# Kernel optimization log

Measured on AMD Instinct MI355X. Metric: run time of the kernel, lower is better.

Reference implementation:

```python
import jax, jax.numpy as jnp
import numpy as np

D_MODEL = 1024
N_HEADS = 16
D_HEAD = D_MODEL // N_HEADS
B, S = 4, 2048


def setup_inputs() -> dict:
    key = jax.random.key(0)
    ks = jax.random.split(key, 12)
    std = 1.0 / np.sqrt(D_MODEL)
    inp = {
        "q": jax.random.normal(ks[0], (B, S, D_MODEL), jnp.float32),
        "k": jax.random.normal(ks[1], (B, S, D_MODEL), jnp.float32),
        "v": jax.random.normal(ks[2], (B, S, D_MODEL), jnp.float32),
        # causal mask: 1 where attention is disallowed (j > i)
        "mask": jnp.triu(jnp.ones((S, S), jnp.int32), k=1)[None, None],
        "Wq": jax.random.normal(ks[3], (D_MODEL, D_MODEL), jnp.float32) * std,
        "bq": jnp.zeros((D_MODEL,), jnp.float32),
        "Wk": jax.random.normal(ks[4], (D_MODEL, D_MODEL), jnp.float32) * std,
        "bk": jnp.zeros((D_MODEL,), jnp.float32),
        "Wv": jax.random.normal(ks[5], (D_MODEL, D_MODEL), jnp.float32) * std,
        "bv": jnp.zeros((D_MODEL,), jnp.float32),
        "Wo": jax.random.normal(ks[6], (D_MODEL, D_MODEL), jnp.float32) * std,
        "bo": jnp.zeros((D_MODEL,), jnp.float32),
    }
    return inp


def _split_heads(x):
    # [B, S, D] -> [B, H, S, d_head]
    b, s, _ = x.shape
    return x.reshape(b, s, N_HEADS, D_HEAD).transpose(0, 2, 1, 3)


def reference(q, k, v, mask, Wq, bq, Wk, bk, Wv, bv, Wo, bo):
    # torch Linear: y = x @ W.T + b
    qh = _split_heads(q @ Wq.T + bq)
    kh = _split_heads(k @ Wk.T + bk)
    vh = _split_heads(v @ Wv.T + bv)
    # NOTE: original scales by sqrt(d_model), not sqrt(d_head)
    scale = 1.0 / np.sqrt(D_MODEL).astype(np.float32)
    logits = jnp.einsum("bhqd,bhkd->bhqk", qh, kh) * scale
    logits = logits + mask.astype(logits.dtype) * (-1e9)
    weights = jax.nn.softmax(logits, axis=-1)
    attn = jnp.einsum("bhqk,bhkd->bhqd", weights, vh)
    attn = attn.transpose(0, 2, 1, 3).reshape(q.shape[0], -1, D_MODEL)
    out = attn @ Wo.T + bo
    return out, weights
```

## Files before the change

### kernel.cpp

```cpp
#include <hip/hip_runtime.h>
#include <stdint.h>

typedef unsigned short u16;
typedef __attribute__((ext_vector_type(8))) short bf16x8;
typedef __attribute__((ext_vector_type(8))) unsigned short us8;
typedef __attribute__((ext_vector_type(4))) float f32x4;

typedef __attribute__((address_space(1))) void as1_void;
typedef __attribute__((address_space(3))) void as3_void;

#define S_LEN 2048
#define DMODEL 1024
#define DH 64
#define NHEADS 16
#define NB 4
#define GM (NB * S_LEN)
#define GN DMODEL
#define GK DMODEL
#define SCALE 0.03125f

__device__ __forceinline__ void gload16(const void* g, void* l) {
  __builtin_amdgcn_global_load_lds((const as1_void*)g, (as3_void*)l, 16, 0, 0);
}
__device__ __forceinline__ float bf2f(u16 u) {
  union { unsigned int i; float f; } x; x.i = ((unsigned int)u) << 16; return x.f;
}
__device__ __forceinline__ u16 f2bf(float f) {
  union { float f; unsigned int i; } x; x.f = f;
  unsigned int u = x.i + 0x7fffu + ((x.i >> 16) & 1u);
  return (u16)(u >> 16);
}
__device__ __forceinline__ f32x4 mfma16(bf16x8 a, bf16x8 b, f32x4 c) {
  return __builtin_amdgcn_mfma_f32_16x16x32_bf16(a, b, c, 0, 0, 0);
}
__device__ __forceinline__ void nt_store4(f32x4 v, float* p) {
  __builtin_nontemporal_store(v, (f32x4*)p);
}

__device__ __forceinline__ void cvt_chunk(const float* s, u16* d, int i) {
  const f32x4 a = *(const f32x4*)(s + (size_t)i * 8);
  const f32x4 b = *(const f32x4*)(s + (size_t)i * 8 + 4);
  us8 o;
  o[0] = f2bf(a[0]); o[1] = f2bf(a[1]); o[2] = f2bf(a[2]); o[3] = f2bf(a[3]);
  o[4] = f2bf(b[0]); o[5] = f2bf(b[1]); o[6] = f2bf(b[2]); o[7] = f2bf(b[3]);
  *(us8*)(d + (size_t)i * 8) = o;
}
__global__ __launch_bounds__(256)
void cvt3(const float* __restrict__ s0, const float* __restrict__ s1,
          const float* __restrict__ s2, u16* __restrict__ d0,
          u16* __restrict__ d1, u16* __restrict__ d2, int n8) {
  const int i = blockIdx.x * 256 + threadIdx.x;
  if (i >= n8) return;
  const float* s; u16* d;
  if (blockIdx.y == 0)      { s = s0; d = d0; }
  else if (blockIdx.y == 1) { s = s1; d = d1; }
  else                      { s = s2; d = d2; }
  cvt_chunk(s, d, i);
}
__global__ __launch_bounds__(256)
void cvt4(const float* __restrict__ s0, const float* __restrict__ s1,
          const float* __restrict__ s2, const float* __restrict__ s3,
          u16* __restrict__ d0, u16* __restrict__ d1,
          u16* __restrict__ d2, u16* __restrict__ d3, int n8) {
  const int i = blockIdx.x * 256 + threadIdx.x;
  if (i >= n8) return;
  const float* s; u16* d;
  if (blockIdx.y == 0)      { s = s0; d = d0; }
  else if (blockIdx.y == 1) { s = s1; d = d1; }
  else if (blockIdx.y == 2) { s = s2; d = d2; }
  else                      { s = s3; d = d3; }
  cvt_chunk(s, d, i);
}

__device__ __forceinline__ void zero_tiles(float* __restrict__ wz, int tid,
                                           int t0, int bh_base, int tmax,
                                           int stride) {
  const f32x4 z4 = {0.f, 0.f, 0.f, 0.f};
  for (int t = t0; t < tmax; t += stride) {
    const int bh = bh_base + t / 120;
    int r = t % 120;
    int i = 0;
    while (r >= 15 - i) { r -= 15 - i; ++i; }
    const int j = i + 1 + r;
    float* p = wz + ((size_t)(bh * 2048 + i * 128)) * 2048 + j * 128;
#pragma unroll 4
    for (int c = tid; c < 4096; c += 256)
      nt_store4(z4, p + (size_t)(c >> 5) * 2048 + ((c & 31) << 2));
  }
}

#define GEMM_IDX                                                              \
  const int tid  = threadIdx.x;                                               \
  const int lane = tid & 63;                                                  \
  const int wvi  = tid >> 6;                                                  \
  const int wr   = wvi >> 1, wc = wvi & 1;                                    \
  const int rlow = lane & 15, rhi = lane >> 4;

#define GEMM_COMPUTE(Ab, Bb)                                                  \
  {                                                                           \
    bf16x8 af[4][2], bfr[4][2];                                               \
    _Pragma("unroll")                                                         \
    for (int mi = 0; mi < 4; ++mi) {                                          \
      const int row = wr * 64 + mi * 16 + rlow;                               \
      _Pragma("unroll")                                                       \
      for (int k2 = 0; k2 < 2; ++k2)                                          \
        af[mi][k2] = *(const bf16x8*)&(Ab)[row * 64 +                         \
                     (((rhi + k2 * 4) ^ (row & 7)) << 3)];                    \
    }                                                                         \
    _Pragma("unroll")                                                         \
    for (int ni = 0; ni < 4; ++ni) {                                          \
      const int row = wc * 64 + ni * 16 + rlow;                               \
      _Pragma("unroll")                                                       \
      for (int k2 = 0; k2 < 2; ++k2)                                          \
        bfr[ni][k2] = *(const bf16x8*)&(Bb)[row * 64 +                        \
                      (((rhi + k2 * 4) ^ (row & 7)) << 3)];                   \
    }                                                                         \
    _Pragma("unroll")                                                         \
    for (int mi = 0; mi < 4; ++mi)                                            \
      _Pragma("unroll")                                                       \
      for (int ni = 0; ni < 4; ++ni) {                                        \
        acc[mi][ni] = mfma16(af[mi][0], bfr[ni][0], acc[mi][ni]);             \
        acc[mi][ni] = mfma16(af[mi][1], bfr[ni][1], acc[mi][ni]);             \
      }                                                                       \
  }

#define ZSPLIT 5800

__global__ __launch_bounds__(256, 3)
void gemm_qkv(const u16* __restrict__ xq, const u16* __restrict__ xk,
              const u16* __restrict__ xv, const u16* __restrict__ wq,
              const u16* __restrict__ wk, const u16* __restrict__ wv,
              const float* __restrict__ bq, const float* __restrict__ bk,
              const float* __restrict__ bv, u16* __restrict__ oq,
              u16* __restrict__ ok, u16* __restrict__ ov,
              float* __restrict__ wz) {
  __shared__ u16 smem[2 * 8192];
  u16* As = smem;
  u16* Bs = smem + 8192;
  const u16 *A, *W; const float* bias; u16* C;
  if (blockIdx.z == 0)      { A = xq; W = wq; bias = bq; C = oq; }
  else if (blockIdx.z == 1) { A = xk; W = wk; bias = bk; C = ok; }
  else                      { A = xv; W = wv; bias = bv; C = ov; }
  GEMM_IDX
  const int m0 = blockIdx.x * 128;
  const int n0 = blockIdx.y * 128;

  f32x4 acc[4][4];
#pragma unroll
  for (int i = 0; i < 4; ++i)
#pragma unroll
    for (int j = 0; j < 4; ++j) acc[i][j] = (f32x4){0.f, 0.f, 0.f, 0.f};

  const int nk = GK >> 6;
  for (int kk = 0; kk < nk; ++kk) {
#pragma unroll
    for (int i = 0; i < 4; ++i) {
      const int c = i * 256 + tid;
      const int row = c >> 3, cw = c & 7;
      const int koff = (kk << 6) + ((cw ^ (row & 7)) << 3);
      gload16(A + (size_t)(m0 + row) * GK + koff, &As[(c - lane) << 3]);
      gload16(W + (size_t)(n0 + row) * GK + koff, &Bs[(c - lane) << 3]);
    }
    __syncthreads();
    GEMM_COMPUTE(As, Bs)
    __syncthreads();
  }

  {
    u16* Cs = smem;
#pragma unroll
    for (int ni = 0; ni < 4; ++ni) {
      const int col = wc * 64 + ni * 16 + rlow;
      const float bv2 = bias[n0 + col];
#pragma unroll
      for (int mi = 0; mi < 4; ++mi)
#pragma unroll
        for (int r = 0; r < 4; ++r)
          Cs[(wr * 64 + mi * 16 + rhi * 4 + r) * 128 + col] = f2bf(acc[mi][ni][r] + bv2);
    }
    __syncthreads();
#pragma unroll
    for (int i = 0; i < 8; ++i) {
      const int c = i * 256 + tid;
      const int row = c >> 4, cw = c & 15;
      const us8 t = *(const us8*)&Cs[row * 128 + cw * 8];
      *(us8*)&C[(size_t)(m0 + row) * GN + n0 + cw * 8] = t;
    }
  }

  {
    const int fid = blockIdx.x + blockIdx.y * 64 + blockIdx.z * 512;
    zero_tiles(wz, tid, fid, 3, ZSPLIT, 1536);
  }
}

__global__ __launch_bounds__(256, 2)
void gemm_o(const u16* __restrict__ A, const u16* __restrict__ W,
            const float* __restrict__ bias, float* __restrict__ C,
            float* __restrict__ wz) {
  __shared__ u16 smem[4 * 8192];
  u16* As = smem;
  u16* Bs = smem + 2 * 8192;
  GEMM_IDX
  const int m0 = blockIdx.x * 128;
  const int n0 = blockIdx.y * 128;

  f32x4 acc[4][4];
#pragma unroll
  for (int i = 0; i < 4; ++i)
#pragma unroll
    for (int j = 0; j < 4; ++j) acc[i][j] = (f32x4){0.f, 0.f, 0.f, 0.f};

#define STAGE_G(bufi, kk)                                                     \
  {                                                                           \
    _Pragma("unroll")                                                         \
    for (int i = 0; i < 4; ++i) {                                             \
      const int c = i * 256 + tid;                                            \
      const int row = c >> 3, cw = c & 7;                                     \
      const int koff = ((kk) << 6) + ((cw ^ (row & 7)) << 3);                 \
      gload16(A + (size_t)(m0 + row) * GK + koff,                             \
              &As[(bufi) * 8192 + ((c - lane) << 3)]);                        \
      gload16(W + (size_t)(n0 + row) * GK + koff,                             \
              &Bs[(bufi) * 8192 + ((c - lane) << 3)]);                        \
    }                                                                         \
  }

  const int nk = GK >> 6;
  STAGE_G(0, 0);
  __syncthreads();
  int buf = 0;
  for (int kk = 0; kk < nk; ++kk) {
    if (kk + 1 < nk) STAGE_G(buf ^ 1, kk + 1);
    const u16* Ab = &As[buf * 8192];
    const u16* Bb = &Bs[buf * 8192];
    GEMM_COMPUTE(Ab, Bb)
    __syncthreads();
    buf ^= 1;
  }
#undef STAGE_G

  {
    float* Cs = (float*)smem;
#pragma unroll
    for (int ni = 0; ni < 4; ++ni) {
      const int col = wc * 64 + ni * 16 + rlow;
      const float bv2 = bias[n0 + col];
#pragma unroll
      for (int mi = 0; mi < 4; ++mi)
#pragma unroll
        for (int r = 0; r < 4; ++r)
          Cs[(wr * 64 + mi * 16 + rhi * 4 + r) * 128 + col] = acc[mi][ni][r] + bv2;
    }
    __syncthreads();
#pragma unroll
    for (int i = 0; i < 16; ++i) {
      const int c = i * 256 + tid;
      const int row = c >> 5, cw = c & 31;
      const f32x4 t = *(const f32x4*)&Cs[row * 128 + cw * 4];
      nt_store4(t, &C[(size_t)(m0 + row) * GN + n0 + cw * 4]);
    }
  }

  {
    const int fid = blockIdx.x + blockIdx.y * 64;
    zero_tiles(wz, tid, ZSPLIT + fid, 3, 7320, 512);
    zero_tiles(wz, tid, fid, 0, 360, 512);
  }
}

__global__ __launch_bounds__(512, 4)
void attn_fused(const u16* __restrict__ qh, const u16* __restrict__ kh,
                const u16* __restrict__ vh, float* __restrict__ wout,
                u16* __restrict__ am)
{
  __shared__ u16 smem[34304];
  u16* Ws  = smem;
  u16* Qs  = smem;
  u16* Kb1 = smem;
  u16* Kb0 = smem + 17408;
  u16* VT  = smem + 17408 + 8192;

  const int tid = threadIdx.x, lane = tid & 63, wv = tid >> 6;
  const int rlow = lane & 15, rhi = lane >> 4;
  const int idx = blockIdx.x;
  const int bh  = idx & 63;
  const int qt  = 15 - (idx >> 6);
  const int b = bh >> 4, h = bh & 15;
  const int q0 = qt << 7;
  const size_t headoff = (size_t)b * S_LEN * DMODEL + h * DH;

#define STAGE_K(dst, jtile)                                                   \
  {                                                                           \
    _Pragma("unroll")                                                         \
    for (int i = 0; i < 2; ++i) {                                             \
      const int c = i * 512 + tid;                                            \
      const int row = c >> 3, cw = c & 7;                                     \
      gload16(kh + headoff + (size_t)((jtile) * 128 + row) * DMODEL +         \
              ((cw ^ (row & 7)) << 3), &(dst)[(c - lane) << 3]);              \
    }                                                                         \
  }
#define LOAD_V(jtile)                                                         \
  {                                                                           \
    const int d0v = wv << 3;                                                  \
    vvA = *(const bf16x8*)(vh + headoff +                                     \
          (size_t)((jtile) * 128 + lane) * DMODEL + d0v);                     \
    vvB = *(const bf16x8*)(vh + headoff +                                     \
          (size_t)((jtile) * 128 + 64 + lane) * DMODEL + d0v);                \
  }

#pragma unroll
  for (int i = 0; i < 2; ++i) {
    const int c = i * 512 + tid;
    const int row = c >> 3, cw = c & 7;
    gload16(qh + headoff + (size_t)(q0 + row) * DMODEL + ((cw ^ (row & 7)) << 3),
            &Qs[(c - lane) << 3]);
  }
  __syncthreads();
  bf16x8 qf[2];
  {
    const int row = wv * 16 + rlow;
#pragma unroll
    for (int k2 = 0; k2 < 2; ++k2)
      qf[k2] = *(const bf16x8*)&Qs[row * 64 + (((rhi + k2 * 4) ^ (row & 7)) << 3)];
  }

  const int gi_base = q0 + wv * 16 + rhi * 4;
  float ssum[4] = {0.f, 0.f, 0.f, 0.f};

  STAGE_K(Kb0, 0);
  for (int jt = 0; jt <= qt; ++jt) {
    __syncthreads();
    const u16* kcur = (jt & 1) ? Kb1 : Kb0;
    if (jt < qt) {
      u16* knxt = (jt & 1) ? Kb0 : Kb1;
      STAGE_K(knxt, jt + 1);
    }
    const bool diag = (jt == qt);
    float pexp[4] = {0.f, 0.f, 0.f, 0.f};
#pragma unroll
    for (int half = 0; half < 2; ++half) {
      f32x4 acc[4];
#pragma unroll
      for (int ni = 0; ni < 4; ++ni) acc[ni] = (f32x4){0.f, 0.f, 0.f, 0.f};
#pragma unroll
      for (int k2 = 0; k2 < 2; ++k2) {
#pragma unroll
        for (int ni = 0; ni < 4; ++ni) {
          const int row = (half * 4 + ni) * 16 + rlow;
          bf16x8 kf = *(const bf16x8*)&kcur[row * 64 + (((rhi + k2 * 4) ^ (row & 7)) << 3)];
          acc[ni] = mfma16(qf[k2], kf, acc[ni]);
        }
      }
#pragma unroll
      for (int ni = 0; ni < 4; ++ni) {
        const int gj = jt * 128 + (half * 4 + ni) * 16 + rlow;
#pragma unroll
        for (int r = 0; r < 4; ++r) {
          if (!diag || gj <= gi_base + r) pexp[r] += __expf(acc[ni][r] * SCALE);
        }
      }
    }
#pragma unroll
    for (int r = 0; r < 4; ++r) {
      float p = pexp[r];
      p += __shfl_xor(p, 1);
      p += __shfl_xor(p, 2);
      p += __shfl_xor(p, 4);
      p += __shfl_xor(p, 8);
      ssum[r] += p;
    }
  }
  float inv_s[4];
#pragma unroll
  for (int r = 0; r < 4; ++r) inv_s[r] = 1.f / ssum[r];

  f32x4 opv[4];
#pragma unroll
  for (int ni = 0; ni < 4; ++ni) opv[ni] = (f32x4){0.f, 0.f, 0.f, 0.f};

  bf16x8 vvA, vvB;
  __syncthreads();
  STAGE_K(Kb0, 0);
  LOAD_V(0);
  __syncthreads();

  for (int jt = 0; jt <= qt; ++jt) {
    {
      const int d0v = wv << 3;
#pragma unroll
      for (int e = 0; e < 8; ++e) {
        VT[(d0v + e) * 136 + lane] = (u16)vvA[e];
        VT[(d0v + e) * 136 + 64 + lane] = (u16)vvB[e];
      }
    }
    const bool diag = (jt == qt);
#pragma unroll
    for (int half = 0; half < 2; ++half) {
      f32x4 acc[4];
#pragma unroll
      for (int ni = 0; ni < 4; ++ni) acc[ni] = (f32x4){0.f, 0.f, 0.f, 0.f};
#pragma unroll
      for (int k2 = 0; k2 < 2; ++k2) {
#pragma unroll
        for (int ni = 0; ni < 4; ++ni) {
          const int row = (half * 4 + ni) * 16 + rlow;
          bf16x8 kf = *(const bf16x8*)&Kb0[row * 64 + (((rhi + k2 * 4) ^ (row & 7)) << 3)];
          acc[ni] = mfma16(qf[k2], kf, acc[ni]);
        }
      }
#pragma unroll
      for (int ni = 0; ni < 4; ++ni) {
        const int col = (half * 4 + ni) * 16 + rlow;
        const int gj = jt * 128 + col;
#pragma unroll
        for (int r = 0; r < 4; ++r) {
          float w = 0.f;
          if (!diag || gj <= gi_base + r) w = __expf(acc[ni][r] * SCALE) * inv_s[r];
          Ws[(wv * 16 + rhi * 4 + r) * 136 + col] = f2bf(w);
        }
      }
    }
    asm volatile("s_waitcnt lgkmcnt(0)" ::: "memory");
    __builtin_amdgcn_s_barrier();
    __builtin_amdgcn_sched_barrier(0);
    if (jt < qt) {
      STAGE_K(Kb0, jt + 1);
      LOAD_V(jt + 1);
    }
    {
      const size_t wbase = ((size_t)bh * S_LEN + q0) * S_LEN + (size_t)jt * 128;
#pragma unroll
      for (int i = 0; i < 8; ++i) {
        const int c = i * 512 + tid;
        const int row = c >> 5, cw = c & 31;
        f32x4 t;
        t[0] = bf2f(Ws[row * 136 + cw * 4 + 0]);
        t[1] = bf2f(Ws[row * 136 + cw * 4 + 1]);
        t[2] = bf2f(Ws[row * 136 + cw * 4 + 2]);
        t[3] = bf2f(Ws[row * 136 + cw * 4 + 3]);
        nt_store4(t, wout + wbase + (size_t)row * S_LEN + cw * 4);
      }
    }
#pragma unroll
    for (int k4 = 0; k4 < 4; ++k4) {
      const bf16x8 afr = *(const bf16x8*)&Ws[(wv * 16 + rlow) * 136 + rhi * 8 + k4 * 32];
#pragma unroll
      for (int ni = 0; ni < 4; ++ni) {
        const bf16x8 vfr = *(const bf16x8*)&VT[(ni * 16 + rlow) * 136 + rhi * 8 + k4 * 32];
        opv[ni] = mfma16(afr, vfr, opv[ni]);
      }
    }
    asm volatile("s_waitcnt vmcnt(8) lgkmcnt(0)" ::: "memory");
    __builtin_amdgcn_s_barrier();
    __builtin_amdgcn_sched_barrier(0);
  }
#undef STAGE_K
#undef LOAD_V

  {
    u16* Os = smem;
#pragma unroll
    for (int ni = 0; ni < 4; ++ni)
#pragma unroll
      for (int r = 0; r < 4; ++r)
        Os[(wv * 16 + rhi * 4 + r) * 72 + ni * 16 + rlow] = f2bf(opv[ni][r]);
    __syncthreads();
#pragma unroll
    for (int i = 0; i < 2; ++i) {
      const int c = i * 512 + tid;
      const int row = c >> 3, cw = c & 7;
      const us8 t = *(const us8*)&Os[row * 72 + cw * 8];
      *(us8*)(am + headoff + (size_t)(q0 + row) * DMODEL + cw * 8) = t;
    }
  }
}

extern "C" void kernel_launch(void* const* d_in, const int* in_sizes, int n_in,
                              void* d_out, int out_size, void* d_ws, size_t ws_size,
                              hipStream_t stream) {
  const float* q  = (const float*)d_in[0];
  const float* k  = (const float*)d_in[1];
  const float* v  = (const float*)d_in[2];
  const float* Wq = (const float*)d_in[4];
  const float* bq = (const float*)d_in[5];
  const float* Wk = (const float*)d_in[6];
  const float* bk = (const float*)d_in[7];
  const float* Wv = (const float*)d_in[8];
  const float* bv = (const float*)d_in[9];
  const float* Wo = (const float*)d_in[10];
  const float* bo = (const float*)d_in[11];

  const size_t proj_elems = (size_t)NB * S_LEN * DMODEL;
  const size_t w_elems    = (size_t)DMODEL * DMODEL;
  float* out0 = (float*)d_out;
  float* wts  = out0 + proj_elems;

  u16* qh  = (u16*)d_ws;
  u16* kh  = qh + proj_elems;
  u16* vh  = kh + proj_elems;
  u16* am  = vh + proj_elems;
  u16* wco = am + proj_elems;

  u16* xq = (u16*)wts;
  u16* xk = xq + proj_elems;
  u16* xv = xk + proj_elems;
  u16* wq_ = (u16*)out0;
  u16* wk_ = wq_ + w_elems;
  u16* wv_ = wk_ + w_elems;

  const int n8x = (int)(proj_elems / 8);
  const int n8w = (int)(w_elems / 8);

  cvt3<<<dim3(n8x / 256, 3), dim3(256), 0, stream>>>(q, k, v, xq, xk, xv, n8x);
  cvt4<<<dim3(n8w / 256, 4), dim3(256), 0, stream>>>(Wq, Wk, Wv, Wo,
                                                     wq_, wk_, wv_, wco, n8w);
  gemm_qkv<<<dim3(64, 8, 3), dim3(256), 0, stream>>>(xq, xk, xv, wq_, wk_, wv_,
                                                     bq, bk, bv, qh, kh, vh, wts);
  attn_fused<<<dim3(1024), dim3(512), 0, stream>>>(qh, kh, vh, wts, am);
  gemm_o<<<dim3(64, 8), dim3(256), 0, stream>>>(am, wco, bo, out0, wts);
}
```

Before: 328.9 us.

## Halve attention query tile to 64 rows and split key columns across wave pairs

The attention kernel now handles 64 query rows per block instead of 128, and doubles the grid to 2048 blocks. Within a block, waves are split into 4 row groups by 2 key-column halves, with partial softmax sums combined through shared memory. Shared memory shrinks and the occupancy hint rises from 4 to 6 blocks to improve load balance and latency hiding on the causal triangle. In exchange, K and V tiles are loaded twice as often per query row, an extra barrier is added, and the diagonal tile of odd query tiles wastes half its work.

```diff
diff --git a/kernel.cpp b/kernel.cpp
--- a/kernel.cpp
+++ b/kernel.cpp
@@ -268,25 +268,29 @@
   }
 }
 
-__global__ __launch_bounds__(512, 4)
+__global__ __launch_bounds__(512, 6)
 void attn_fused(const u16* __restrict__ qh, const u16* __restrict__ kh,
                 const u16* __restrict__ vh, float* __restrict__ wout,
                 u16* __restrict__ am)
 {
-  __shared__ u16 smem[34304];
+  __shared__ u16 smem[25600];
   u16* Ws  = smem;
   u16* Qs  = smem;
   u16* Kb1 = smem;
-  u16* Kb0 = smem + 17408;
-  u16* VT  = smem + 17408 + 8192;
+  float* sbuf = (float*)&smem[8192];
+  u16* Kb0 = smem + 8704;
+  u16* VT  = smem + 16896;
 
   const int tid = threadIdx.x, lane = tid & 63, wv = tid >> 6;
   const int rlow = lane & 15, rhi = lane >> 4;
+  const int rg = wv & 3;
+  const int jh = wv >> 2;
   const int idx = blockIdx.x;
   const int bh  = idx & 63;
-  const int qt  = 15 - (idx >> 6);
+  const int qt  = 31 - (idx >> 6);
   const int b = bh >> 4, h = bh & 15;
-  const int q0 = qt << 7;
+  const int q0 = qt << 6;
+  const int jtmax = qt >> 1;
   const size_t headoff = (size_t)b * S_LEN * DMODEL + h * DH;
 
 #define STAGE_K(dst, jtile)                                                   \
@@ -308,9 +312,8 @@
           (size_t)((jtile) * 128 + 64 + lane) * DMODEL + d0v);                \
   }
 
-#pragma unroll
-  for (int i = 0; i < 2; ++i) {
-    const int c = i * 512 + tid;
+  {
+    const int c = tid;
     const int row = c >> 3, cw = c & 7;
     gload16(qh + headoff + (size_t)(q0 + row) * DMODEL + ((cw ^ (row & 7)) << 3),
             &Qs[(c - lane) << 3]);
@@ -318,46 +321,43 @@
   __syncthreads();
   bf16x8 qf[2];
   {
-    const int row = wv * 16 + rlow;
+    const int qrow = rg * 16 + rlow;
 #pragma unroll
     for (int k2 = 0; k2 < 2; ++k2)
-      qf[k2] = *(const bf16x8*)&Qs[row * 64 + (((rhi + k2 * 4) ^ (row & 7)) << 3)];
-  }
-
-  const int gi_base = q0 + wv * 16 + rhi * 4;
+      qf[k2] = *(const bf16x8*)&Qs[qrow * 64 + (((rhi + k2 * 4) ^ (qrow & 7)) << 3)];
+  }
+
+  const int gi_base = q0 + rg * 16 + rhi * 4;
   float ssum[4] = {0.f, 0.f, 0.f, 0.f};
 
   STAGE_K(Kb0, 0);
-  for (int jt = 0; jt <= qt; ++jt) {
+  for (int jt = 0; jt <= jtmax; ++jt) {
     __syncthreads();
     const u16* kcur = (jt & 1) ? Kb1 : Kb0;
-    if (jt < qt) {
+    if (jt < jtmax) {
       u16* knxt = (jt & 1) ? Kb0 : Kb1;
       STAGE_K(knxt, jt + 1);
     }
-    const bool diag = (jt == qt);
+    const bool diag = (jt == jtmax);
     float pexp[4] = {0.f, 0.f, 0.f, 0.f};
-#pragma unroll
-    for (int half = 0; half < 2; ++half) {
-      f32x4 acc[4];
-#pragma unroll
-      for (int ni = 0; ni < 4; ++ni) acc[ni] = (f32x4){0.f, 0.f, 0.f, 0.f};
-#pragma unroll
-      for (int k2 = 0; k2 < 2; ++k2) {
-#pragma unroll
-        for (int ni = 0; ni < 4; ++ni) {
-          const int row = (half * 4 + ni) * 16 + rlow;
-          bf16x8 kf = *(const bf16x8*)&kcur[row * 64 + (((rhi + k2 * 4) ^ (row & 7)) << 3)];
-          acc[ni] = mfma16(qf[k2], kf, acc[ni]);
-        }
-      }
+    f32x4 acc[4];
+#pragma unroll
+    for (int ni = 0; ni < 4; ++ni) acc[ni] = (f32x4){0.f, 0.f, 0.f, 0.f};
+#pragma unroll
+    for (int k2 = 0; k2 < 2; ++k2) {
 #pragma unroll
       for (int ni = 0; ni < 4; ++ni) {
-        const int gj = jt * 128 + (half * 4 + ni) * 16 + rlow;
-#pragma unroll
-        for (int r = 0; r < 4; ++r) {
-          if (!diag || gj <= gi_base + r) pexp[r] += __expf(acc[ni][r] * SCALE);
-        }
+        const int row = (jh * 4 + ni) * 16 + rlow;
+        bf16x8 kf = *(const bf16x8*)&kcur[row * 64 + (((rhi + k2 * 4) ^ (row & 7)) << 3)];
+        acc[ni] = mfma16(qf[k2], kf, acc[ni]);
+      }
+    }
+#pragma unroll
+    for (int ni = 0; ni < 4; ++ni) {
+      const int gj = jt * 128 + (jh * 4 + ni) * 16 + rlow;
+#pragma unroll
+      for (int r = 0; r < 4; ++r) {
+        if (!diag || gj <= gi_base + r) pexp[r] += __expf(acc[ni][r] * SCALE);
       }
     }
 #pragma unroll
@@ -370,21 +370,28 @@
       ssum[r] += p;
     }
   }
+  if (rlow == 0) {
+#pragma unroll
+    for (int r = 0; r < 4; ++r) sbuf[jh * 64 + rg * 16 + rhi * 4 + r] = ssum[r];
+  }
+  __syncthreads();
   float inv_s[4];
 #pragma unroll
-  for (int r = 0; r < 4; ++r) inv_s[r] = 1.f / ssum[r];
-
-  f32x4 opv[4];
-#pragma unroll
-  for (int ni = 0; ni < 4; ++ni) opv[ni] = (f32x4){0.f, 0.f, 0.f, 0.f};
+  for (int r = 0; r < 4; ++r) {
+    const int row = rg * 16 + rhi * 4 + r;
+    inv_s[r] = 1.f / (sbuf[row] + sbuf[64 + row]);
+  }
+
+  f32x4 opv[2];
+#pragma unroll
+  for (int ni = 0; ni < 2; ++ni) opv[ni] = (f32x4){0.f, 0.f, 0.f, 0.f};
 
   bf16x8 vvA, vvB;
-  __syncthreads();
   STAGE_K(Kb0, 0);
   LOAD_V(0);
   __syncthreads();
 
-  for (int jt = 0; jt <= qt; ++jt) {
+  for (int jt = 0; jt <= jtmax; ++jt) {
     {
       const int d0v = wv << 3;
 #pragma unroll
@@ -393,9 +400,8 @@
         VT[(d0v + e) * 136 + 64 + lane] = (u16)vvB[e];
       }
     }
-    const bool diag = (jt == qt);
-#pragma unroll
-    for (int half = 0; half < 2; ++half) {
+    const bool diag = (jt == jtmax);
+    {
       f32x4 acc[4];
 #pragma unroll
       for (int ni = 0; ni < 4; ++ni) acc[ni] = (f32x4){0.f, 0.f, 0.f, 0.f};
@@ -403,34 +409,34 @@
       for (int k2 = 0; k2 < 2; ++k2) {
 #pragma unroll
         for (int ni = 0; ni < 4; ++ni) {
-          const int row = (half * 4 + ni) * 16 + rlow;
+          const int row = (jh * 4 + ni) * 16 + rlow;
           bf16x8 kf = *(const bf16x8*)&Kb0[row * 64 + (((rhi + k2 * 4) ^ (row & 7)) << 3)];
           acc[ni] = mfma16(qf[k2], kf, acc[ni]);
         }
       }
 #pragma unroll
       for (int ni = 0; ni < 4; ++ni) {
-        const int col = (half * 4 + ni) * 16 + rlow;
+        const int col = (jh * 4 + ni) * 16 + rlow;
         const int gj = jt * 128 + col;
 #pragma unroll
         for (int r = 0; r < 4; ++r) {
           float w = 0.f;
           if (!diag || gj <= gi_base + r) w = __expf(acc[ni][r] * SCALE) * inv_s[r];
-          Ws[(wv * 16 + rhi * 4 + r) * 136 + col] = f2bf(w);
+          Ws[(rg * 16 + rhi * 4 + r) * 136 + col] = f2bf(w);
         }
       }
     }
     asm volatile("s_waitcnt lgkmcnt(0)" ::: "memory");
     __builtin_amdgcn_s_barrier();
     __builtin_amdgcn_sched_barrier(0);
-    if (jt < qt) {
+    if (jt < jtmax) {
       STAGE_K(Kb0, jt + 1);
       LOAD_V(jt + 1);
     }
     {
       const size_t wbase = ((size_t)bh * S_LEN + q0) * S_LEN + (size_t)jt * 128;
 #pragma unroll
-      for (int i = 0; i < 8; ++i) {
+      for (int i = 0; i < 4; ++i) {
         const int c = i * 512 + tid;
         const int row = c >> 5, cw = c & 31;
         f32x4 t;
@@ -443,14 +449,14 @@
     }
 #pragma unroll
     for (int k4 = 0; k4 < 4; ++k4) {
-      const bf16x8 afr = *(const bf16x8*)&Ws[(wv * 16 + rlow) * 136 + rhi * 8 + k4 * 32];
-#pragma unroll
-      for (int ni = 0; ni < 4; ++ni) {
-        const bf16x8 vfr = *(const bf16x8*)&VT[(ni * 16 + rlow) * 136 + rhi * 8 + k4 * 32];
+      const bf16x8 afr = *(const bf16x8*)&Ws[(rg * 16 + rlow) * 136 + rhi * 8 + k4 * 32];
+#pragma unroll
+      for (int ni = 0; ni < 2; ++ni) {
+        const bf16x8 vfr = *(const bf16x8*)&VT[((jh * 2 + ni) * 16 + rlow) * 136 + rhi * 8 + k4 * 32];
         opv[ni] = mfma16(afr, vfr, opv[ni]);
       }
     }
-    asm volatile("s_waitcnt vmcnt(8) lgkmcnt(0)" ::: "memory");
+    asm volatile("s_waitcnt vmcnt(4) lgkmcnt(0)" ::: "memory");
     __builtin_amdgcn_s_barrier();
     __builtin_amdgcn_sched_barrier(0);
   }
@@ -460,14 +466,13 @@
   {
     u16* Os = smem;
 #pragma unroll
-    for (int ni = 0; ni < 4; ++ni)
+    for (int ni = 0; ni < 2; ++ni)
 #pragma unroll
       for (int r = 0; r < 4; ++r)
-        Os[(wv * 16 + rhi * 4 + r) * 72 + ni * 16 + rlow] = f2bf(opv[ni][r]);
-    __syncthreads();
-#pragma unroll
-    for (int i = 0; i < 2; ++i) {
-      const int c = i * 512 + tid;
+        Os[(rg * 16 + rhi * 4 + r) * 72 + (jh * 2 + ni) * 16 + rlow] = f2bf(opv[ni][r]);
+    __syncthreads();
+    {
+      const int c = tid;
       const int row = c >> 3, cw = c & 7;
       const us8 t = *(const us8*)&Os[row * 72 + cw * 8];
       *(us8*)(am + headoff + (size_t)(q0 + row) * DMODEL + cw * 8) = t;
@@ -516,6 +521,6 @@
                                                      wq_, wk_, wv_, wco, n8w);
   gemm_qkv<<<dim3(64, 8, 3), dim3(256), 0, stream>>>(xq, xk, xv, wq_, wk_, wv_,
                                                      bq, bk, bv, qh, kh, vh, wts);
-  attn_fused<<<dim3(1024), dim3(512), 0, stream>>>(qh, kh, vh, wts, am);
+  attn_fused<<<dim3(2048), dim3(512), 0, stream>>>(qh, kh, vh, wts, am);
   gemm_o<<<dim3(64, 8), dim3(256), 0, stream>>>(am, wco, bo, out0, wts);
 }
```

Result: slower. 364.2 us (+10.7%).
